# Performance work log

Measured on AMD Instinct MI355X. Metric: run time of the kernel, lower is better.

## Reference

```python
import jax, jax.numpy as jnp
import numpy as np

N_BINS = 64
EPS = 0.001
T_MIN = 0.0
T_MAX = 1.0


def setup_inputs() -> dict:
    key = jax.random.key(0)
    k_t, k_lt, k_lu = jax.random.split(key, 3)
    t = jax.random.uniform(k_t, (32, 4096), dtype=jnp.float32)
    # learned per-bin logits, initialized like torch (zeros - log(n_bins)) plus noise
    base = -jnp.float32(np.log(N_BINS))
    l_t = base + 0.1 * jax.random.normal(k_lt, (N_BINS,), dtype=jnp.float32)
    l_u = base + 0.1 * jax.random.normal(k_lu, (N_BINS,), dtype=jnp.float32)
    return {"t": t, "l_t": l_t, "l_u": l_u}


def reference(t, l_t, l_u):
    # Per-bin weights (params are shared across all (n,l) positions, so compute once
    # on the 1-D bin axis and broadcast -- same math as expanding first).
    w_t = jax.nn.softmax(l_t) + EPS
    w_t = w_t / jnp.sum(w_t)
    w_u = jnp.exp(l_u) + EPS
    w_u = w_u / jnp.sum(w_u)  # normalized=True

    zero = jnp.zeros((1,), dtype=w_t.dtype)
    e_t = jnp.concatenate([zero, jnp.cumsum(w_t)])  # [n_bins+1]
    e_u = jnp.concatenate([zero, jnp.cumsum(w_u)])  # [n_bins+1]

    t_prime = (t - T_MIN) / (T_MAX - T_MIN)  # [n, l]
    # bucket search: count knots <= t', then clamp
    idx = jnp.sum((e_t[None, None, :] <= t_prime[:, :, None]).astype(jnp.int32), axis=-1) - 1
    idx = jnp.clip(idx, 0, N_BINS - 1)  # [n, l]

    et0 = e_t[idx]
    et1 = e_t[idx + 1]
    eu0 = e_u[idx]
    eu1 = e_u[idx + 1]
    u = eu0 + (eu1 - eu0) * ((t_prime - et0) / (et1 - et0))
    return u
```

## Files before the change

### kernel.cpp

```cpp
#include <hip/hip_runtime.h>
#include <math.h>

#define N_BINS 64
#define EPS_W 0.001f
#define LUT_SIZE 256

__device__ inline float wave_sum(float v) {
    #pragma unroll
    for (int off = 32; off >= 1; off >>= 1) v += __shfl_xor(v, off, 64);
    return v;
}
__device__ inline float wave_max(float v) {
    #pragma unroll
    for (int off = 32; off >= 1; off >>= 1) v = fmaxf(v, __shfl_xor(v, off, 64));
    return v;
}
__device__ inline float wave_scan_incl(float v, int lane) {
    #pragma unroll
    for (int off = 1; off < 64; off <<= 1) {
        float o = __shfl_up(v, off, 64);
        if (lane >= off) v += o;
    }
    return v;
}

__global__ __launch_bounds__(256) void losscdf_kernel(
    const float* __restrict__ t,
    const float* __restrict__ l_t,
    const float* __restrict__ l_u,
    float* __restrict__ out,
    int n)
{
    __shared__ float  s_et[N_BINS + 1];
    __shared__ float4 s_bin[N_BINS];
    __shared__ int    s_lut[LUT_SIZE];

    if (threadIdx.x < 64) {
        int lane = threadIdx.x;
        float lt = l_t[lane];
        float lu = l_u[lane];

        float m  = wave_max(lt);
        float ex = expf(lt - m);
        float se = wave_sum(ex);
        float wt = ex / se + EPS_W;
        float swt = wave_sum(wt);
        wt = wt / swt;

        float eu = expf(lu) + EPS_W;
        float seu = wave_sum(eu);
        float wu = eu / seu;

        float ct = wave_scan_incl(wt, lane);
        float cu = wave_scan_incl(wu, lane);

        if (lane == 0) s_et[0] = 0.0f;
        s_et[lane + 1] = ct;

        float et0 = ct - wt;
        float et1 = ct;
        float eu0 = cu - wu;
        float eu1 = cu;
        if (lane == 0) { et0 = 0.0f; eu0 = 0.0f; }
        float4 b;
        b.x = et0;
        b.y = eu0;
        b.z = (eu1 - eu0) / (et1 - et0);
        b.w = et1;
        s_bin[lane] = b;
    }
    __syncthreads();

    {
        float slot_lo = (float)threadIdx.x * (1.0f / LUT_SIZE);
        int idx = 0;
        #pragma unroll
        for (int s = 32; s; s >>= 1) {
            int cand = idx + s;
            idx = (s_et[cand] <= slot_lo) ? cand : idx;
        }
        s_lut[threadIdx.x] = idx;
    }
    __syncthreads();

    int i = blockIdx.x * blockDim.x + threadIdx.x;
    if (i < n) {
        float tp = t[i];
        int k = (int)(tp * (float)LUT_SIZE);
        k = min(max(k, 0), LUT_SIZE - 1);
        int idx = s_lut[k];
        while (idx < N_BINS - 1 && s_et[idx + 1] <= tp) idx++;
        float4 b = s_bin[idx];
        out[i] = fmaf(b.z, tp - b.x, b.y);
    }
}

extern "C" void kernel_launch(void* const* d_in, const int* in_sizes, int n_in,
                              void* d_out, int out_size, void* d_ws, size_t ws_size,
                              hipStream_t stream) {
    const float* t   = (const float*)d_in[0];
    const float* l_t = (const float*)d_in[1];
    const float* l_u = (const float*)d_in[2];
    float* out = (float*)d_out;
    int n = in_sizes[0];
    int block = 256;
    int grid = (n + block - 1) / block;
    if (grid < 1) grid = 1;
    losscdf_kernel<<<grid, block, 0, stream>>>(t, l_t, l_u, out, n);
}
```

Measured before the change: 58.09 us.

## Use single-wave blocks with float4 elements and barrier-free LUT construction

Each block is now one 64-lane wavefront, and each lane processes four elements through float4 loads and stores. The input load is issued before the per-block softmax and scan so its latency overlaps that setup. The LUT is built by each bin lane filling its own slot range, which removes both __syncthreads barriers and the per-slot binary search. The cost is a less uniform LUT fill loop per lane, plus reliance on in-wave LDS visibility without an explicit barrier.

```diff
diff --git a/kernel.cpp b/kernel.cpp
--- a/kernel.cpp
+++ b/kernel.cpp
@@ -1,9 +1,11 @@
 #include <hip/hip_runtime.h>
 #include <math.h>
 
-#define N_BINS 64
-#define EPS_W 0.001f
+#define N_BINS   64
+#define EPS_W    0.001f
 #define LUT_SIZE 256
+#define BLOCK    64
+#define VEC      4
 
 __device__ inline float wave_sum(float v) {
     #pragma unroll
@@ -24,74 +26,83 @@
     return v;
 }
 
-__global__ __launch_bounds__(256) void losscdf_kernel(
+__device__ inline float lookup_one(const float4* __restrict__ bin,
+                                   const int*    __restrict__ lut,
+                                   float tp)
+{
+    int k = (int)(tp * (float)LUT_SIZE);
+    k = min(max(k, 0), LUT_SIZE - 1);
+    int idx = lut[k];
+    idx = min(max(idx, 0), N_BINS - 1);
+    float4 b = bin[idx];
+    while (idx > 0 && b.x > tp)            b = bin[--idx];
+    while (idx < N_BINS - 1 && b.w <= tp)  b = bin[++idx];
+    return fmaf(b.z, tp - b.x, b.y);
+}
+
+__global__ __launch_bounds__(BLOCK) void losscdf_kernel(
     const float* __restrict__ t,
     const float* __restrict__ l_t,
     const float* __restrict__ l_u,
     float* __restrict__ out,
     int n)
 {
-    __shared__ float  s_et[N_BINS + 1];
     __shared__ float4 s_bin[N_BINS];
     __shared__ int    s_lut[LUT_SIZE];
 
-    if (threadIdx.x < 64) {
-        int lane = threadIdx.x;
-        float lt = l_t[lane];
-        float lu = l_u[lane];
+    const int lane = threadIdx.x;
 
-        float m  = wave_max(lt);
-        float ex = expf(lt - m);
-        float se = wave_sum(ex);
-        float wt = ex / se + EPS_W;
-        float swt = wave_sum(wt);
-        wt = wt / swt;
+    const int  gi   = blockIdx.x * BLOCK + lane;
+    const long base = (long)gi * VEC;
+    const bool full = (base + VEC <= (long)n);
+    float4 tp4 = make_float4(0.f, 0.f, 0.f, 0.f);
+    if (full) tp4 = reinterpret_cast<const float4*>(t)[gi];
 
-        float eu = expf(lu) + EPS_W;
-        float seu = wave_sum(eu);
-        float wu = eu / seu;
+    float lt = l_t[lane];
+    float lu = l_u[lane];
 
-        float ct = wave_scan_incl(wt, lane);
-        float cu = wave_scan_incl(wu, lane);
+    float m   = wave_max(lt);
+    float ex  = expf(lt - m);
+    float se  = wave_sum(ex);
+    float wt  = ex / se + EPS_W;
+    float swt = wave_sum(wt);
+    wt = wt / swt;
 
-        if (lane == 0) s_et[0] = 0.0f;
-        s_et[lane + 1] = ct;
+    float eu  = expf(lu) + EPS_W;
+    float seu = wave_sum(eu);
+    float wu  = eu / seu;
 
-        float et0 = ct - wt;
-        float et1 = ct;
-        float eu0 = cu - wu;
-        float eu1 = cu;
-        if (lane == 0) { et0 = 0.0f; eu0 = 0.0f; }
-        float4 b;
-        b.x = et0;
-        b.y = eu0;
-        b.z = (eu1 - eu0) / (et1 - et0);
-        b.w = et1;
-        s_bin[lane] = b;
-    }
-    __syncthreads();
+    float ct = wave_scan_incl(wt, lane);
+    float cu = wave_scan_incl(wu, lane);
 
-    {
-        float slot_lo = (float)threadIdx.x * (1.0f / LUT_SIZE);
-        int idx = 0;
-        #pragma unroll
-        for (int s = 32; s; s >>= 1) {
-            int cand = idx + s;
-            idx = (s_et[cand] <= slot_lo) ? cand : idx;
-        }
-        s_lut[threadIdx.x] = idx;
-    }
-    __syncthreads();
+    float et1 = ct;
+    float et0 = ct - wt;
+    float eu0 = cu - wu;
+    if (lane == 0) { et0 = 0.0f; eu0 = 0.0f; }
 
-    int i = blockIdx.x * blockDim.x + threadIdx.x;
-    if (i < n) {
-        float tp = t[i];
-        int k = (int)(tp * (float)LUT_SIZE);
-        k = min(max(k, 0), LUT_SIZE - 1);
-        int idx = s_lut[k];
-        while (idx < N_BINS - 1 && s_et[idx + 1] <= tp) idx++;
-        float4 b = s_bin[idx];
-        out[i] = fmaf(b.z, tp - b.x, b.y);
+    float4 b;
+    b.x = et0;
+    b.y = eu0;
+    b.z = (cu - eu0) / (et1 - et0);
+    b.w = et1;
+    s_bin[lane] = b;
+
+    int k0 = (int)ceilf(et0 * (float)LUT_SIZE);
+    int k1 = (int)ceilf(et1 * (float)LUT_SIZE);
+    k0 = max(k0, 0);
+    k1 = (lane == N_BINS - 1) ? LUT_SIZE : min(k1, LUT_SIZE);
+    for (int k = k0; k < k1; ++k) s_lut[k] = lane;
+
+    if (full) {
+        float4 r;
+        r.x = lookup_one(s_bin, s_lut, tp4.x);
+        r.y = lookup_one(s_bin, s_lut, tp4.y);
+        r.z = lookup_one(s_bin, s_lut, tp4.z);
+        r.w = lookup_one(s_bin, s_lut, tp4.w);
+        reinterpret_cast<float4*>(out)[gi] = r;
+    } else if (base < (long)n) {
+        for (long e = base; e < (long)n; ++e)
+            out[e] = lookup_one(s_bin, s_lut, t[e]);
     }
 }
 
@@ -103,8 +114,7 @@
     const float* l_u = (const float*)d_in[2];
     float* out = (float*)d_out;
     int n = in_sizes[0];
-    int block = 256;
-    int grid = (n + block - 1) / block;
+    int grid = (n + BLOCK * VEC - 1) / (BLOCK * VEC);
     if (grid < 1) grid = 1;
-    losscdf_kernel<<<grid, block, 0, stream>>>(t, l_t, l_u, out, n);
+    losscdf_kernel<<<grid, BLOCK, 0, stream>>>(t, l_t, l_u, out, n);
 }
```

After: 57.97 us. No clear change (-0.2%).
